# Kernel tuning notes

Hardware: AMD Instinct MI355X
Metric: run time of the kernel (lower is better)

Reference implementation:

```python
import jax, jax.numpy as jnp
import numpy as np

B, D_IN, H = 16384, 512, 1024


def setup_inputs() -> dict:
    key = jax.random.key(0)
    ks = jax.random.split(key, 12)
    s_in = 1.0 / np.sqrt(D_IN)
    s_h = 1.0 / np.sqrt(H)
    d = {
        "input_x": jax.random.normal(ks[0], (B, D_IN), jnp.float32),
        "h_old": jax.random.normal(ks[1], (B, H), jnp.float32),
        "c_old": jax.random.normal(ks[2], (B, H), jnp.float32),
    }
    names_U = ["Ui", "Uf", "Uo", "Uc"]
    names_W = ["Wi", "Wf", "Wo", "Wc"]
    for i, n in enumerate(names_U):
        d[n + "_w"] = jax.random.normal(ks[3 + i], (D_IN, H), jnp.float32) * s_in
        d[n + "_b"] = jnp.zeros((H,), jnp.float32)
    for i, n in enumerate(names_W):
        d[n + "_w"] = jax.random.normal(ks[7 + i], (H, H), jnp.float32) * s_h
        d[n + "_b"] = jnp.zeros((H,), jnp.float32)
    return d


def reference(input_x, h_old, c_old,
              Ui_w, Ui_b, Wi_w, Wi_b,
              Uf_w, Uf_b, Wf_w, Wf_b,
              Uo_w, Uo_b, Wo_w, Wo_b,
              Uc_w, Uc_b, Wc_w, Wc_b):
    # Fuse the 8 small GEMMs into 2: concatenate gate projections along the
    # output dim (math identical to 8 separate Dense layers + adds).
    U = jnp.concatenate([Ui_w, Uf_w, Uo_w, Uc_w], axis=1)   # [D_in, 4H]
    W = jnp.concatenate([Wi_w, Wf_w, Wo_w, Wc_w], axis=1)   # [H, 4H]
    b = jnp.concatenate([Ui_b + Wi_b, Uf_b + Wf_b, Uo_b + Wo_b, Uc_b + Wc_b])
    gates = input_x @ U + h_old @ W + b                      # [B, 4H]
    i_t, f_t, o_t, g_t = jnp.split(gates, 4, axis=1)
    i_t = jax.nn.sigmoid(i_t)
    f_t = jax.nn.sigmoid(f_t)
    o_t = jax.nn.sigmoid(o_t)
    c_t = jnp.tanh(g_t)
    c = i_t * c_t + f_t * c_old
    h_new = o_t * jnp.tanh(c)
    return (h_new, c)
```

## Files before the change

### kernel.cpp

```cpp
#include <hip/hip_runtime.h>
#include <hip/hip_bf16.h>
#include <stdint.h>

#define B_ROWS 16384
#define D_IN   512
#define H_DIM  1024
#define K_TOT  1536
#define NKT    48

typedef __attribute__((ext_vector_type(8)))  short bf16x8;
typedef __attribute__((ext_vector_type(4)))  float f32x4;
typedef __attribute__((ext_vector_type(4)))  float float4v;
typedef __attribute__((ext_vector_type(8)))  unsigned short u16x8;

__device__ __forceinline__ unsigned short f2bf(float f) {
    uint32_t u = __float_as_uint(f);
    u = (u + 0x7FFFu + ((u >> 16) & 1u)) >> 16;
    return (unsigned short)u;
}

__global__ void cvt_A(const float* __restrict__ x, const float* __restrict__ h,
                      unsigned short* __restrict__ Ag) {
    int t     = blockIdx.x * blockDim.x + threadIdx.x;
    int lane  = t & 63;
    int chunk = (t >> 6) & 15;
    int rest  = t >> 10;
    int T     = rest % 48;
    int bm    = rest / 48;
    int row   = bm * 256 + chunk * 16 + (lane & 15);
    int k     = T * 32 + (lane >> 4) * 8;
    const float* src = (k < 512) ? (x + (size_t)row * D_IN + k)
                                 : (h + (size_t)row * H_DIM + (k - 512));
    float4v v0 = *(const float4v*)(src);
    float4v v1 = *(const float4v*)(src + 4);
    u16x8 o;
    o[0] = f2bf(v0[0]); o[1] = f2bf(v0[1]); o[2] = f2bf(v0[2]); o[3] = f2bf(v0[3]);
    o[4] = f2bf(v1[0]); o[5] = f2bf(v1[1]); o[6] = f2bf(v1[2]); o[7] = f2bf(v1[3]);
    *(u16x8*)(Ag + (size_t)t * 8) = o;
}

__global__ void cvt_B(const float* __restrict__ Ui, const float* __restrict__ Uf,
                      const float* __restrict__ Uo, const float* __restrict__ Uc,
                      const float* __restrict__ Wi, const float* __restrict__ Wf,
                      const float* __restrict__ Wo, const float* __restrict__ Wc,
                      unsigned short* __restrict__ Bg) {
    int t     = blockIdx.x * blockDim.x + threadIdx.x;
    int lane  = t & 63;
    int chunk = (t >> 6) & 15;
    int rest  = t >> 10;
    int T     = rest % 48;
    int bn    = rest / 48;
    int c     = bn * 256 + chunk * 16 + (lane & 15);
    int g     = (c >> 4) & 3;
    int hcol  = ((c >> 6) << 4) | (c & 15);
    int k     = T * 32 + (lane >> 4) * 8;
    const float* up = (g == 0) ? Ui : (g == 1) ? Uf : (g == 2) ? Uo : Uc;
    const float* wp = (g == 0) ? Wi : (g == 1) ? Wf : (g == 2) ? Wo : Wc;
    u16x8 o;
    if (k < 512) {
        const float* s = up + (size_t)k * H_DIM + hcol;
        #pragma unroll
        for (int i = 0; i < 8; ++i) o[i] = f2bf(s[(size_t)i * H_DIM]);
    } else {
        const float* s = wp + (size_t)(k - 512) * H_DIM + hcol;
        #pragma unroll
        for (int i = 0; i < 8; ++i) o[i] = f2bf(s[(size_t)i * H_DIM]);
    }
    *(u16x8*)(Bg + (size_t)t * 8) = o;
}

__global__ void cvt_bias(const float* __restrict__ Uib, const float* __restrict__ Ufb,
                         const float* __restrict__ Uob, const float* __restrict__ Ucb,
                         const float* __restrict__ Wib, const float* __restrict__ Wfb,
                         const float* __restrict__ Wob, const float* __restrict__ Wcb,
                         float* __restrict__ bias) {
    int t = blockIdx.x * blockDim.x + threadIdx.x;
    int g = t >> 10, h = t & 1023;
    const float* ub = (g == 0) ? Uib : (g == 1) ? Ufb : (g == 2) ? Uob : Ucb;
    const float* wb = (g == 0) ? Wib : (g == 1) ? Wfb : (g == 2) ? Wob : Wcb;
    bias[t] = ub[h] + wb[h];
}

__global__ __launch_bounds__(512) void lstm_gemm(
        const unsigned short* __restrict__ Ag, const unsigned short* __restrict__ Bg,
        const float* __restrict__ bias, const float* __restrict__ c_old,
        float* __restrict__ out) {
    __shared__ __align__(1024) char lds[163840];

    const int tid = threadIdx.x;
    const int l   = tid & 63;
    const int wv  = tid >> 6;
    const int wm  = wv >> 2;
    const int wn  = wv & 3;

    const int orig = blockIdx.x;
    const int xcd  = orig & 7;
    const int jj   = orig >> 3;
    const int bn   = (xcd & 3) * 4 + (jj & 3);
    const int bm   = (xcd >> 2) * 32 + (jj >> 2);

    const unsigned short* aSrc = Ag + (size_t)bm * 48 * 8192 + (size_t)(2 * wv) * 512 + l * 8;
    const unsigned short* bSrc = Bg + (size_t)bn * 48 * 8192 + (size_t)(2 * wv) * 512 + l * 8;

    const int aRd = wm * 8192 + l * 16;
    const int bRd = 16384 + wn * 4096 + l * 16;

#define GLDS(SRC, DST) __builtin_amdgcn_global_load_lds(                            \
        (const __attribute__((address_space(1))) void*)(SRC),                       \
        (__attribute__((address_space(3))) void*)(DST), 16, 0, 0)

#define STAGE_T(T, SLOTBASE) do {                                                   \
    const unsigned short* _sa = aSrc + (size_t)(T) * 8192;                          \
    const unsigned short* _sb = bSrc + (size_t)(T) * 8192;                          \
    char* _d = (char*)lds + (SLOTBASE) + wv * 2048;                                 \
    GLDS(_sa, _d);          GLDS(_sa + 512, _d + 1024);                             \
    GLDS(_sb, _d + 16384);  GLDS(_sb + 512, _d + 16384 + 1024);                     \
} while (0)

    f32x4 acc[8][4] = {};

    STAGE_T(0, 0);
    STAGE_T(1, 32768);
    STAGE_T(2, 65536);
    asm volatile("s_waitcnt vmcnt(4)");
    __builtin_amdgcn_s_barrier();

    int rdBase = 0;
    int ssBase = 98304;

    #pragma unroll 1
    for (int t = 0; t < NKT; ++t) {
        int ts = t + 3; if (ts >= NKT) ts -= NKT;

        const char* _A = (const char*)lds + rdBase + aRd;
        const char* _B = (const char*)lds + rdBase + bRd;
        bf16x8 aF[8], bF[4];
        #pragma unroll
        for (int i = 0; i < 8; ++i)
            aF[i] = *(const bf16x8*)(_A + i * 1024);
        #pragma unroll
        for (int n = 0; n < 4; ++n)
            bF[n] = *(const bf16x8*)(_B + n * 1024);

        STAGE_T(ts, ssBase);

        __builtin_amdgcn_s_setprio(1);
        #pragma unroll
        for (int i = 0; i < 8; ++i)
            #pragma unroll
            for (int n = 0; n < 4; ++n)
                acc[i][n] = __builtin_amdgcn_mfma_f32_16x16x32_bf16(
                    aF[i], bF[n], acc[i][n], 0, 0, 0);
        __builtin_amdgcn_s_setprio(0);

        asm volatile("s_waitcnt vmcnt(4)");
        __builtin_amdgcn_s_barrier();

        rdBase = (rdBase == 131072) ? 0 : rdBase + 32768;
        ssBase = (ssBase == 131072) ? 0 : ssBase + 32768;
    }
    asm volatile("s_waitcnt vmcnt(0)");

    const int hh  = (bn * 4 + wn) * 16 + (l & 15);
    const float bi  = bias[hh];
    const float bff = bias[1024 + hh];
    const float bo  = bias[2048 + hh];
    const float bc  = bias[3072 + hh];

    #pragma unroll
    for (int a = 0; a < 8; ++a) {
        const int rb = bm * 256 + wm * 128 + (a >> 2) * 64 + (a & 3) * 16 + ((l >> 4) * 4);
        #pragma unroll
        for (int j = 0; j < 4; ++j) {
            const int r = rb + j;
            float iv = acc[a][0][j] + bi;
            float fv = acc[a][1][j] + bff;
            float ov = acc[a][2][j] + bo;
            float gv = acc[a][3][j] + bc;
            float it = 1.f / (1.f + __expf(-iv));
            float ft = 1.f / (1.f + __expf(-fv));
            float ot = 1.f / (1.f + __expf(-ov));
            float gt = 1.f - 2.f / (1.f + __expf(2.f * gv));
            float co = c_old[(size_t)r * H_DIM + hh];
            float cn = it * gt + ft * co;
            float th = 1.f - 2.f / (1.f + __expf(2.f * cn));
            out[(size_t)r * H_DIM + hh] = ot * th;
            out[(size_t)B_ROWS * H_DIM + (size_t)r * H_DIM + hh] = cn;
        }
    }
#undef STAGE_T
#undef GLDS
}

extern "C" void kernel_launch(void* const* d_in, const int* in_sizes, int n_in,
                              void* d_out, int out_size, void* d_ws, size_t ws_size,
                              hipStream_t stream) {
    const float* x  = (const float*)d_in[0];
    const float* h0 = (const float*)d_in[1];
    const float* c0 = (const float*)d_in[2];
    const float* Uw[4] = {(const float*)d_in[3],  (const float*)d_in[5],
                          (const float*)d_in[7],  (const float*)d_in[9]};
    const float* Ub[4] = {(const float*)d_in[4],  (const float*)d_in[6],
                          (const float*)d_in[8],  (const float*)d_in[10]};
    const float* Ww[4] = {(const float*)d_in[11], (const float*)d_in[13],
                          (const float*)d_in[15], (const float*)d_in[17]};
    const float* Wb[4] = {(const float*)d_in[12], (const float*)d_in[14],
                          (const float*)d_in[16], (const float*)d_in[18]};

    unsigned short* Ag = (unsigned short*)d_ws;
    unsigned short* Bg = Ag + (size_t)B_ROWS * K_TOT;
    float* bias        = (float*)(Bg + (size_t)4096 * K_TOT);
    float* out         = (float*)d_out;

    cvt_A<<<12288, 256, 0, stream>>>(x, h0, Ag);
    cvt_B<<<3072, 256, 0, stream>>>(Uw[0], Uw[1], Uw[2], Uw[3],
                                    Ww[0], Ww[1], Ww[2], Ww[3], Bg);
    cvt_bias<<<16, 256, 0, stream>>>(Ub[0], Ub[1], Ub[2], Ub[3],
                                     Wb[0], Wb[1], Wb[2], Wb[3], bias);
    lstm_gemm<<<1024, 512, 0, stream>>>(Ag, Bg, bias, c0, out);
}
```

Baseline: 257.7 us.

## Load A fragments directly from global into registers, stage only B via LDS

```diff
diff --git a/kernel.cpp b/kernel.cpp
--- a/kernel.cpp
+++ b/kernel.cpp
@@ -85,7 +85,7 @@
         const unsigned short* __restrict__ Ag, const unsigned short* __restrict__ Bg,
         const float* __restrict__ bias, const float* __restrict__ c_old,
         float* __restrict__ out) {
-    __shared__ __align__(1024) char lds[163840];
+    __shared__ __align__(1024) char lds[81920];
 
     const int tid = threadIdx.x;
     const int l   = tid & 63;
@@ -99,65 +99,72 @@
     const int bn   = (xcd & 3) * 4 + (jj & 3);
     const int bm   = (xcd >> 2) * 32 + (jj >> 2);
 
-    const unsigned short* aSrc = Ag + (size_t)bm * 48 * 8192 + (size_t)(2 * wv) * 512 + l * 8;
-    const unsigned short* bSrc = Bg + (size_t)bn * 48 * 8192 + (size_t)(2 * wv) * 512 + l * 8;
-
-    const int aRd = wm * 8192 + l * 16;
-    const int bRd = 16384 + wn * 4096 + l * 16;
+    const unsigned short* aBase =
+        Ag + ((size_t)bm * 48 * 16 + wm * 8) * 512 + l * 8;
+    const unsigned short* bSrc =
+        Bg + ((size_t)bn * 48 * 16 + 2 * wv) * 512 + l * 8;
+    const int bRd = wn * 4096 + l * 16;
 
 #define GLDS(SRC, DST) __builtin_amdgcn_global_load_lds(                            \
         (const __attribute__((address_space(1))) void*)(SRC),                       \
         (__attribute__((address_space(3))) void*)(DST), 16, 0, 0)
 
-#define STAGE_T(T, SLOTBASE) do {                                                   \
-    const unsigned short* _sa = aSrc + (size_t)(T) * 8192;                          \
-    const unsigned short* _sb = bSrc + (size_t)(T) * 8192;                          \
+#define STAGE_B(T, SLOTBASE) do {                                                   \
+    const unsigned short* _s = bSrc + (size_t)(T) * 8192;                           \
     char* _d = (char*)lds + (SLOTBASE) + wv * 2048;                                 \
-    GLDS(_sa, _d);          GLDS(_sa + 512, _d + 1024);                             \
-    GLDS(_sb, _d + 16384);  GLDS(_sb + 512, _d + 16384 + 1024);                     \
+    GLDS(_s, _d);  GLDS(_s + 512, _d + 1024);                                       \
 } while (0)
 
+#define ALOAD(AF, T) do {                                                           \
+    const unsigned short* _a = aBase + (size_t)(T) * 8192;                          \
+    AF[0] = *(const u16x8*)(_a);        AF[1] = *(const u16x8*)(_a + 512);          \
+    AF[2] = *(const u16x8*)(_a + 1024); AF[3] = *(const u16x8*)(_a + 1536);         \
+    AF[4] = *(const u16x8*)(_a + 2048); AF[5] = *(const u16x8*)(_a + 2560);         \
+    AF[6] = *(const u16x8*)(_a + 3072); AF[7] = *(const u16x8*)(_a + 3584);         \
+} while (0)
+
     f32x4 acc[8][4] = {};
 
-    STAGE_T(0, 0);
-    STAGE_T(1, 32768);
-    STAGE_T(2, 65536);
-    asm volatile("s_waitcnt vmcnt(4)");
+#define TILE(AC, AN, T, RD, SS) do {                                                \
+    const char* _B = (const char*)lds + (RD) + bRd;                                 \
+    bf16x8 bF[4];                                                                   \
+    _Pragma("unroll") for (int n = 0; n < 4; ++n)                                   \
+        bF[n] = *(const bf16x8*)(_B + n * 1024);                                    \
+    int _tn = (T) + 1; if (_tn >= NKT) _tn = 0;        \
+    ALOAD(AN, _tn);                                                                 \
+    int _ts = (T) + 3; if (_ts >= NKT) _ts -= NKT;    \
+    STAGE_B(_ts, SS);                                                               \
+    __builtin_amdgcn_s_setprio(1);                                                  \
+    _Pragma("unroll") for (int i = 0; i < 8; ++i)                                   \
+        _Pragma("unroll") for (int n = 0; n < 4; ++n)                               \
+            acc[i][n] = __builtin_amdgcn_mfma_f32_16x16x32_bf16(                    \
+                (bf16x8)AC[i], bF[n], acc[i][n], 0, 0, 0);                          \
+    __builtin_amdgcn_s_setprio(0);                                                  \
+    asm volatile("s_waitcnt vmcnt(2)");                                             \
+    __builtin_amdgcn_s_barrier();                                                   \
+} while (0)
+
+    u16x8 aP[8], aQ[8];
+
+    ALOAD(aP, 0);
+    STAGE_B(0, 0);
+    STAGE_B(1, 16384);
+    STAGE_B(2, 32768);
+    asm volatile("s_waitcnt vmcnt(2)");
     __builtin_amdgcn_s_barrier();
 
-    int rdBase = 0;
-    int ssBase = 98304;
+    int rdB = 0;
+    int ssB = 49152;
 
     #pragma unroll 1
-    for (int t = 0; t < NKT; ++t) {
-        int ts = t + 3; if (ts >= NKT) ts -= NKT;
-
-        const char* _A = (const char*)lds + rdBase + aRd;
-        const char* _B = (const char*)lds + rdBase + bRd;
-        bf16x8 aF[8], bF[4];
-        #pragma unroll
-        for (int i = 0; i < 8; ++i)
-            aF[i] = *(const bf16x8*)(_A + i * 1024);
-        #pragma unroll
-        for (int n = 0; n < 4; ++n)
-            bF[n] = *(const bf16x8*)(_B + n * 1024);
-
-        STAGE_T(ts, ssBase);
-
-        __builtin_amdgcn_s_setprio(1);
-        #pragma unroll
-        for (int i = 0; i < 8; ++i)
-            #pragma unroll
-            for (int n = 0; n < 4; ++n)
-                acc[i][n] = __builtin_amdgcn_mfma_f32_16x16x32_bf16(
-                    aF[i], bF[n], acc[i][n], 0, 0, 0);
-        __builtin_amdgcn_s_setprio(0);
-
-        asm volatile("s_waitcnt vmcnt(4)");
-        __builtin_amdgcn_s_barrier();
-
-        rdBase = (rdBase == 131072) ? 0 : rdBase + 32768;
-        ssBase = (ssBase == 131072) ? 0 : ssBase + 32768;
+    for (int i = 0; i < 24; ++i) {
+        const int t0 = 2 * i;
+        TILE(aP, aQ, t0, rdB, ssB);
+        rdB = (rdB == 65536) ? 0 : rdB + 16384;
+        ssB = (ssB == 65536) ? 0 : ssB + 16384;
+        TILE(aQ, aP, t0 + 1, rdB, ssB);
+        rdB = (rdB == 65536) ? 0 : rdB + 16384;
+        ssB = (ssB == 65536) ? 0 : ssB + 16384;
     }
     asm volatile("s_waitcnt vmcnt(0)");
 
@@ -169,7 +176,7 @@
 
     #pragma unroll
     for (int a = 0; a < 8; ++a) {
-        const int rb = bm * 256 + wm * 128 + (a >> 2) * 64 + (a & 3) * 16 + ((l >> 4) * 4);
+        const int rb = bm * 256 + wm * 128 + a * 16 + ((l >> 4) * 4);
         #pragma unroll
         for (int j = 0; j < 4; ++j) {
             const int r = rb + j;
@@ -188,7 +195,9 @@
             out[(size_t)B_ROWS * H_DIM + (size_t)r * H_DIM + hh] = cn;
         }
     }
-#undef STAGE_T
+#undef TILE
+#undef ALOAD
+#undef STAGE_B
 #undef GLDS
 }
 
```

Result: slower. 296.1 us (+14.9%).
